# Kernel tuning notes

Measured on AMD Instinct MI355X. Metric: run time of the kernel, lower is better.

## Reference

```python
import jax, jax.numpy as jnp
import numpy as np

IN, H, OUT, R, E, B = 4096, 4096, 4096, 512, 4, 64
TOT = R * IN + H * R + R * H + OUT * R  # 8388608


def setup_inputs() -> dict:
    key = jax.random.key(0)
    ks = jax.random.split(key, 7)
    s = 0.02
    x = jax.random.normal(ks[0], (B, IN), jnp.float32)
    scores = jax.random.uniform(ks[1], (E,), jnp.float32)
    delta = jax.random.normal(ks[2], (E, 1, TOT), jnp.float32) * s
    # single shared expert's base weights (all experts alias the same module)
    W1 = jax.random.normal(ks[3], (R, IN), jnp.float32) * s   # hidden_layer_u.weight
    W2 = jax.random.normal(ks[4], (H, R), jnp.float32) * s    # hidden_layer_v.weight
    W3 = jax.random.normal(ks[5], (R, H), jnp.float32) * s    # output_layer_u.weight
    W4 = jax.random.normal(ks[6], (OUT, R), jnp.float32) * s  # output_layer_v.weight
    return {"x": x, "scores": scores, "delta": delta, "W1": W1, "W2": W2, "W3": W3, "W4": W4}


def reference(x, scores, delta, W1, W2, W3, W4):
    # slice flat per-expert deltas into the four weight deltas
    d = delta[:, 0, :]                                   # [E, TOT]
    j = 0
    d1 = d[:, j:j + R * IN].reshape(E, R, IN); j += R * IN
    d2 = d[:, j:j + H * R].reshape(E, H, R);   j += H * R
    d3 = d[:, j:j + R * H].reshape(E, R, H);   j += R * H
    d4 = d[:, j:j + OUT * R].reshape(E, OUT, R)
    Wa = W1[None] + d1   # [E, R, IN]
    Wb = W2[None] + d2   # [E, H, R]
    Wc = W3[None] + d3   # [E, R, H]
    Wd = W4[None] + d4   # [E, OUT, R]
    h = jnp.einsum('bi,eri->ebr', x, Wa)                 # F.linear with W1+d1
    h = jnp.einsum('ebr,ehr->ebh', h, Wb)                # F.linear with W2+d2
    h = jax.nn.relu(h)
    h = jnp.einsum('ebh,erh->ebr', h, Wc)                # F.linear with W3+d3
    h = jnp.einsum('ebr,eor->ebo', h, Wd)                # F.linear with W4+d4
    return jnp.einsum('ebo,e->bo', h, scores)            # score-weighted sum over experts
```

## Files before the change

### kernel.cpp

```cpp
#include <hip/hip_runtime.h>
#include <hip/hip_bf16.h>

#define E_N 4
#define B_N 64
#define IN_N 4096
#define H_N 4096
#define R_N 512
#define OUT_N 4096
#define TOT_N 8388608

typedef float f32x4 __attribute__((ext_vector_type(4)));
typedef short bf16x8 __attribute__((ext_vector_type(8)));

__device__ __forceinline__ unsigned short f2bf_bits(float f) {
    return __builtin_bit_cast(unsigned short, __float2bfloat16(f));
}
__device__ __forceinline__ float bfbits2f(unsigned short u) {
    return __builtin_bit_cast(float, ((unsigned)u) << 16);
}

__device__ __forceinline__ void stage16(const void* g, void* l) {
    __builtin_amdgcn_global_load_lds(
        (const __attribute__((address_space(1))) void*)g,
        (__attribute__((address_space(3))) void*)l, 16, 0, 0);
}

template<int K_TOT, int N_TOT, int KS, bool A_SHARED, bool RELU, bool OUT_BF16>
__global__ __launch_bounds__(256, 2)
void gemm_layer(const __hip_bfloat16* __restrict__ A, const float* __restrict__ W,
                const float* __restrict__ D, float* __restrict__ OutF,
                __hip_bfloat16* __restrict__ OutB)
{
    constexpr int KCH = K_TOT / KS;
    constexpr int NT = N_TOT / 32;
    constexpr int NTILES = KCH / 64;
    constexpr int BUFSZ = 24576;
    __shared__ __align__(16) char smem[2 * BUFSZ];

    const int bid = blockIdx.x;
    const int ks = bid % KS;
    const int nt = (bid / KS) % NT;
    const int e  = bid / (KS * NT);
    const int tid = threadIdx.x;
    const int l  = tid & 63;
    const int w  = tid >> 6;
    const int wn = w & 1;
    const int wm = w >> 1;
    const int lr = l & 15;
    const int lk = (l >> 4) << 3;

    const float* Wb = W + (size_t)(nt * 32) * K_TOT + ks * KCH;
    const float* Db = D + (size_t)e * TOT_N + (size_t)(nt * 32) * K_TOT + ks * KCH;
    const __hip_bfloat16* Ab = A + (A_SHARED ? (size_t)0 : (size_t)e * B_N * K_TOT)
                                 + ks * KCH;

    const char* gsrc[6];
    int loff[6];
    int kstep[6];
    #pragma unroll
    for (int i = 0; i < 6; ++i) {
        const int q = w * 6 + i;
        if (q < 8) {
            const int off = q * 1024 + l * 16;
            const int row = off >> 8;
            const int kb  = off & 255;
            gsrc[i] = (const char*)(Wb + (size_t)row * K_TOT) + (kb ^ ((row & 7) << 4));
            loff[i] = q * 1024;
            kstep[i] = 4;
        } else if (q < 16) {
            const int c = q - 8;
            const int off = c * 1024 + l * 16;
            const int row = off >> 8;
            const int kb  = off & 255;
            gsrc[i] = (const char*)(Db + (size_t)row * K_TOT) + (kb ^ ((row & 7) << 4));
            loff[i] = 8192 + c * 1024;
            kstep[i] = 4;
        } else {
            const int c = q - 16;
            const int off = c * 1024 + l * 16;
            const int row = off >> 7;
            const int kb  = off & 127;
            gsrc[i] = (const char*)(Ab + (size_t)row * K_TOT) + (kb ^ ((row & 7) << 4));
            loff[i] = 16384 + c * 1024;
            kstep[i] = 2;
        }
    }

    f32x4 acc[2] = {};
    const int wrow = wn * 16 + lr;
    const int wswz = (wrow & 7) << 4;
    const int arow0 = wm * 32 + lr;
    const int aswz = (arow0 & 7) << 4;

    #pragma unroll
    for (int i = 0; i < 6; ++i)
        stage16(gsrc[i], smem + loff[i]);
    __syncthreads();

    for (int t = 0; t < NTILES; ++t) {
        if (t + 1 < NTILES) {
            const int kk = (t + 1) * 64;
            char* b = smem + ((t + 1) & 1) * BUFSZ;
            #pragma unroll
            for (int i = 0; i < 6; ++i)
                stage16(gsrc[i] + kk * kstep[i], b + loff[i]);
        }

        const char* buf = smem + (t & 1) * BUFSZ;
        #pragma unroll
        for (int inner = 0; inner < 2; ++inner) {
            const int b0 = (inner * 32 + lk) * 4;
            const char* wrp = buf + wrow * 256;
            const char* drp = buf + 8192 + wrow * 256;
            f32x4 w0 = *(const f32x4*)(wrp + ((b0)      ^ wswz));
            f32x4 w1 = *(const f32x4*)(wrp + ((b0 + 16) ^ wswz));
            f32x4 d0 = *(const f32x4*)(drp + ((b0)      ^ wswz));
            f32x4 d1 = *(const f32x4*)(drp + ((b0 + 16) ^ wswz));
            f32x4 s0 = w0 + d0;
            f32x4 s1 = w1 + d1;
            bf16x8 bhi, blo;
            #pragma unroll
            for (int j = 0; j < 4; ++j) {
                unsigned short h0 = f2bf_bits(s0[j]);
                bhi[j] = (short)h0;
                blo[j] = (short)f2bf_bits(s0[j] - bfbits2f(h0));
                unsigned short h1 = f2bf_bits(s1[j]);
                bhi[j + 4] = (short)h1;
                blo[j + 4] = (short)f2bf_bits(s1[j] - bfbits2f(h1));
            }
            const int ab = (inner * 32 + lk) * 2;
            #pragma unroll
            for (int mf = 0; mf < 2; ++mf) {
                const int ar = arow0 + mf * 16;
                const char* arp = buf + 16384 + ar * 128;
                bf16x8 af = *(const bf16x8*)(arp + (ab ^ aswz));
                acc[mf] = __builtin_amdgcn_mfma_f32_16x16x32_bf16(af, bhi, acc[mf], 0, 0, 0);
                acc[mf] = __builtin_amdgcn_mfma_f32_16x16x32_bf16(af, blo, acc[mf], 0, 0, 0);
            }
        }
        __syncthreads();
    }

    const int rb = (l >> 4) * 4;
    const int nrow = nt * 32 + wrow;
    #pragma unroll
    for (int j = 0; j < 2; ++j) {
        #pragma unroll
        for (int i = 0; i < 4; ++i) {
            const int row = wm * 32 + j * 16 + rb + i;
            float v = acc[j][i];
            if (RELU) v = fmaxf(v, 0.0f);
            if (OUT_BF16) {
                OutB[(size_t)e * B_N * N_TOT + (size_t)row * N_TOT + nrow] =
                    __float2bfloat16(v);
            } else {
                OutF[(size_t)(e * KS + ks) * B_N * N_TOT + (size_t)row * N_TOT + nrow] = v;
            }
        }
    }
}

template<int KS, int BN>
__global__ __launch_bounds__(256)
void reduce_ks_bf16(const float* __restrict__ P, __hip_bfloat16* __restrict__ H)
{
    const int gt = blockIdx.x * 256 + threadIdx.x;
    const int e = gt / BN;
    const int r = gt - e * BN;
    const float* base = P + (size_t)e * KS * BN + r;
    float s = 0.0f;
    #pragma unroll
    for (int k = 0; k < KS; ++k) s += base[(size_t)k * BN];
    H[gt] = __float2bfloat16(s);
}

__global__ __launch_bounds__(256)
void convert_bf16(const float* __restrict__ X, __hip_bfloat16* __restrict__ Xb)
{
    const int gt = blockIdx.x * 256 + threadIdx.x;
    const int idx = gt * 2;
    const float2 v = *(const float2*)(X + idx);
    const unsigned u = ((unsigned)f2bf_bits(v.y) << 16) | f2bf_bits(v.x);
    *(unsigned*)((char*)Xb + (size_t)idx * 2) = u;
}

__global__ __launch_bounds__(256)
void reduce_experts(const float* __restrict__ P, const float* __restrict__ scores,
                    float* __restrict__ out)
{
    const int gt = blockIdx.x * 256 + threadIdx.x;
    const int idx = gt * 2;
    float2 acc = {0.0f, 0.0f};
    #pragma unroll
    for (int e = 0; e < E_N; ++e) {
        const float2 v = *(const float2*)(P + (size_t)e * (B_N * OUT_N) + idx);
        const float s = scores[e];
        acc.x += s * v.x;
        acc.y += s * v.y;
    }
    *(float2*)(out + idx) = acc;
}

extern "C" void kernel_launch(void* const* d_in, const int* in_sizes, int n_in,
                              void* d_out, int out_size, void* d_ws, size_t ws_size,
                              hipStream_t stream)
{
    const float* x      = (const float*)d_in[0];
    const float* scores = (const float*)d_in[1];
    const float* delta  = (const float*)d_in[2];
    const float* W1     = (const float*)d_in[3];
    const float* W2     = (const float*)d_in[4];
    const float* W3     = (const float*)d_in[5];
    const float* W4     = (const float*)d_in[6];
    float* out = (float*)d_out;

    char* ws = (char*)d_ws;
    __hip_bfloat16* xb  = (__hip_bfloat16*)(ws);
    __hip_bfloat16* h1b = (__hip_bfloat16*)(ws + 524288);
    __hip_bfloat16* h2b = (__hip_bfloat16*)(ws + 786432);
    __hip_bfloat16* h3b = (__hip_bfloat16*)(ws + 2883584);
    float* P1 = (float*)(ws + 3145728);
    float* P3 = (float*)(ws + 7340032);
    float* P4 = (float*)(ws + 11534336);

    const float* d1 = delta;
    const float* d2 = d1 + (size_t)R_N * IN_N;
    const float* d3 = d2 + (size_t)H_N * R_N;
    const float* d4 = d3 + (size_t)R_N * H_N;

    convert_bf16<<<dim3(B_N * IN_N / 2 / 256), dim3(256), 0, stream>>>(x, xb);

    gemm_layer<IN_N, R_N, 8, true, false, false>
        <<<dim3(E_N * (R_N / 32) * 8), dim3(256), 0, stream>>>(xb, W1, d1, P1, nullptr);
    reduce_ks_bf16<8, B_N * R_N>
        <<<dim3(E_N * B_N * R_N / 256), dim3(256), 0, stream>>>(P1, h1b);

    gemm_layer<R_N, H_N, 1, false, true, true>
        <<<dim3(E_N * (H_N / 32)), dim3(256), 0, stream>>>(h1b, W2, d2, nullptr, h2b);

    gemm_layer<H_N, R_N, 8, false, false, false>
        <<<dim3(E_N * (R_N / 32) * 8), dim3(256), 0, stream>>>(h2b, W3, d3, P3, nullptr);
    reduce_ks_bf16<8, B_N * R_N>
        <<<dim3(E_N * B_N * R_N / 256), dim3(256), 0, stream>>>(P3, h3b);

    gemm_layer<R_N, OUT_N, 1, false, false, false>
        <<<dim3(E_N * (OUT_N / 32)), dim3(256), 0, stream>>>(h3b, W4, d4, P4, nullptr);

    reduce_experts<<<dim3(B_N * OUT_N / 2 / 256), dim3(256), 0, stream>>>(P4, scores, out);
}
```

Measured before the change: 51.43 us.

## Fold expert score sum into last layer GEMM over concatenated expert K

Scales each expert's layer-3 activations by its score while reducing split-K partials. The activations are written into a layout where experts are concatenated along K. The last layer then becomes a single GEMM with K=E*R that writes the output directly. This removes the per-expert fp32 partial output buffer and the separate expert-reduction kernel. The trade-off is that only 128 blocks run the last layer, with a longer K loop, which may underuse the GPU, and bf16 rounding of the score-scaled activations changes numerics slightly.

```diff
diff --git a/kernel.cpp b/kernel.cpp
--- a/kernel.cpp
+++ b/kernel.cpp
@@ -160,6 +160,129 @@
     }
 }
 
+__global__ __launch_bounds__(256, 2)
+void gemm_l4(const __hip_bfloat16* __restrict__ A, const float* __restrict__ W,
+             const float* __restrict__ D, float* __restrict__ Out)
+{
+    constexpr int KT = E_N * R_N;
+    constexpr int NTILES = KT / 64;
+    constexpr int BUFSZ = 24576;
+    __shared__ __align__(16) char smem[2 * BUFSZ];
+
+    const int nt = blockIdx.x;
+    const int tid = threadIdx.x;
+    const int l  = tid & 63;
+    const int w  = tid >> 6;
+    const int wn = w & 1;
+    const int wm = w >> 1;
+    const int lr = l & 15;
+    const int lk = (l >> 4) << 3;
+
+    const char* gsrc[6];
+    int loff[6];
+    int cls[6];
+    #pragma unroll
+    for (int i = 0; i < 6; ++i) {
+        const int q = w * 6 + i;
+        if (q < 8) {
+            const int off = q * 1024 + l * 16;
+            const int row = off >> 8;
+            const int kb  = (off & 255) ^ (((off >> 8) & 7) << 4);
+            gsrc[i] = (const char*)(W + (size_t)(nt * 32 + row) * R_N) + kb;
+            loff[i] = q * 1024;
+            cls[i] = 0;
+        } else if (q < 16) {
+            const int c = q - 8;
+            const int off = c * 1024 + l * 16;
+            const int row = off >> 8;
+            const int kb  = (off & 255) ^ (((off >> 8) & 7) << 4);
+            gsrc[i] = (const char*)(D + (size_t)(nt * 32 + row) * R_N) + kb;
+            loff[i] = 8192 + c * 1024;
+            cls[i] = 1;
+        } else {
+            const int c = q - 16;
+            const int off = c * 1024 + l * 16;
+            const int row = off >> 7;
+            const int kb  = (off & 127) ^ (((off >> 7) & 7) << 4);
+            gsrc[i] = (const char*)(A + (size_t)row * KT) + kb;
+            loff[i] = 16384 + c * 1024;
+            cls[i] = 2;
+        }
+    }
+
+    f32x4 acc[2] = {};
+    const int wrow = wn * 16 + lr;
+    const int wswz = (wrow & 7) << 4;
+    const int arow0 = wm * 32 + lr;
+    const int aswz = (arow0 & 7) << 4;
+
+    auto toff = [](int c, int kk) -> size_t {
+        if (c == 0) return (size_t)(kk & 511) * 4;
+        if (c == 1) return ((size_t)(kk >> 9) * (size_t)TOT_N + (kk & 511)) * 4;
+        return (size_t)kk * 2;
+    };
+
+    #pragma unroll
+    for (int i = 0; i < 6; ++i)
+        stage16(gsrc[i] + toff(cls[i], 0), smem + loff[i]);
+    __syncthreads();
+
+    for (int t = 0; t < NTILES; ++t) {
+        if (t + 1 < NTILES) {
+            const int kk = (t + 1) * 64;
+            char* b = smem + ((t + 1) & 1) * BUFSZ;
+            #pragma unroll
+            for (int i = 0; i < 6; ++i)
+                stage16(gsrc[i] + toff(cls[i], kk), b + loff[i]);
+        }
+
+        const char* buf = smem + (t & 1) * BUFSZ;
+        #pragma unroll
+        for (int inner = 0; inner < 2; ++inner) {
+            const int b0 = (inner * 32 + lk) * 4;
+            const char* wrp = buf + wrow * 256;
+            const char* drp = buf + 8192 + wrow * 256;
+            f32x4 w0 = *(const f32x4*)(wrp + ((b0)      ^ wswz));
+            f32x4 w1 = *(const f32x4*)(wrp + ((b0 + 16) ^ wswz));
+            f32x4 d0 = *(const f32x4*)(drp + ((b0)      ^ wswz));
+            f32x4 d1 = *(const f32x4*)(drp + ((b0 + 16) ^ wswz));
+            f32x4 s0 = w0 + d0;
+            f32x4 s1 = w1 + d1;
+            bf16x8 bhi, blo;
+            #pragma unroll
+            for (int j = 0; j < 4; ++j) {
+                unsigned short h0 = f2bf_bits(s0[j]);
+                bhi[j] = (short)h0;
+                blo[j] = (short)f2bf_bits(s0[j] - bfbits2f(h0));
+                unsigned short h1 = f2bf_bits(s1[j]);
+                bhi[j + 4] = (short)h1;
+                blo[j + 4] = (short)f2bf_bits(s1[j] - bfbits2f(h1));
+            }
+            const int ab = (inner * 32 + lk) * 2;
+            #pragma unroll
+            for (int mf = 0; mf < 2; ++mf) {
+                const int ar = arow0 + mf * 16;
+                const char* arp = buf + 16384 + ar * 128;
+                bf16x8 af = *(const bf16x8*)(arp + (ab ^ aswz));
+                acc[mf] = __builtin_amdgcn_mfma_f32_16x16x32_bf16(af, bhi, acc[mf], 0, 0, 0);
+                acc[mf] = __builtin_amdgcn_mfma_f32_16x16x32_bf16(af, blo, acc[mf], 0, 0, 0);
+            }
+        }
+        __syncthreads();
+    }
+
+    const int rb = (l >> 4) * 4;
+    const int nrow = nt * 32 + wrow;
+    #pragma unroll
+    for (int j = 0; j < 2; ++j) {
+        #pragma unroll
+        for (int i = 0; i < 4; ++i) {
+            const int row = wm * 32 + j * 16 + rb + i;
+            Out[(size_t)row * OUT_N + nrow] = acc[j][i];
+        }
+    }
+}
+
 template<int KS, int BN>
 __global__ __launch_bounds__(256)
 void reduce_ks_bf16(const float* __restrict__ P, __hip_bfloat16* __restrict__ H)
@@ -175,6 +298,23 @@
 }
 
 __global__ __launch_bounds__(256)
+void reduce_ks_scaled(const float* __restrict__ P, const float* __restrict__ scores,
+                      __hip_bfloat16* __restrict__ H)
+{
+    const int gt = blockIdx.x * 256 + threadIdx.x;
+    const int e = gt >> 15;
+    const int rem = gt & 32767;
+    const int b = rem >> 9;
+    const int r = rem & 511;
+    const float* base = P + (size_t)e * 8 * 32768 + rem;
+    float s = 0.0f;
+    #pragma unroll
+    for (int k = 0; k < 8; ++k) s += base[(size_t)k * 32768];
+    const float v = scores[e] * __bfloat162float(__float2bfloat16(s));
+    H[(size_t)b * (E_N * R_N) + e * R_N + r] = __float2bfloat16(v);
+}
+
+__global__ __launch_bounds__(256)
 void convert_bf16(const float* __restrict__ X, __hip_bfloat16* __restrict__ Xb)
 {
     const int gt = blockIdx.x * 256 + threadIdx.x;
@@ -182,23 +322,6 @@
     const float2 v = *(const float2*)(X + idx);
     const unsigned u = ((unsigned)f2bf_bits(v.y) << 16) | f2bf_bits(v.x);
     *(unsigned*)((char*)Xb + (size_t)idx * 2) = u;
-}
-
-__global__ __launch_bounds__(256)
-void reduce_experts(const float* __restrict__ P, const float* __restrict__ scores,
-                    float* __restrict__ out)
-{
-    const int gt = blockIdx.x * 256 + threadIdx.x;
-    const int idx = gt * 2;
-    float2 acc = {0.0f, 0.0f};
-    #pragma unroll
-    for (int e = 0; e < E_N; ++e) {
-        const float2 v = *(const float2*)(P + (size_t)e * (B_N * OUT_N) + idx);
-        const float s = scores[e];
-        acc.x += s * v.x;
-        acc.y += s * v.y;
-    }
-    *(float2*)(out + idx) = acc;
 }
 
 extern "C" void kernel_launch(void* const* d_in, const int* in_sizes, int n_in,
@@ -218,10 +341,9 @@
     __hip_bfloat16* xb  = (__hip_bfloat16*)(ws);
     __hip_bfloat16* h1b = (__hip_bfloat16*)(ws + 524288);
     __hip_bfloat16* h2b = (__hip_bfloat16*)(ws + 786432);
-    __hip_bfloat16* h3b = (__hip_bfloat16*)(ws + 2883584);
+    __hip_bfloat16* h3s = (__hip_bfloat16*)(ws + 2883584);
     float* P1 = (float*)(ws + 3145728);
     float* P3 = (float*)(ws + 7340032);
-    float* P4 = (float*)(ws + 11534336);
 
     const float* d1 = delta;
     const float* d2 = d1 + (size_t)R_N * IN_N;
@@ -240,11 +362,7 @@
 
     gemm_layer<H_N, R_N, 8, false, false, false>
         <<<dim3(E_N * (R_N / 32) * 8), dim3(256), 0, stream>>>(h2b, W3, d3, P3, nullptr);
-    reduce_ks_bf16<8, B_N * R_N>
-        <<<dim3(E_N * B_N * R_N / 256), dim3(256), 0, stream>>>(P3, h3b);
-
-    gemm_layer<R_N, OUT_N, 1, false, false, false>
-        <<<dim3(E_N * (OUT_N / 32)), dim3(256), 0, stream>>>(h3b, W4, d4, P4, nullptr);
-
-    reduce_experts<<<dim3(B_N * OUT_N / 2 / 256), dim3(256), 0, stream>>>(P4, scores, out);
-}
+    reduce_ks_scaled<<<dim3(E_N * B_N * R_N / 256), dim3(256), 0, stream>>>(P3, scores, h3s);
+
+    gemm_l4<<<dim3(OUT_N / 32), dim3(256), 0, stream>>>(h3s, W4, d4, out);
+}
```

After: 63.82 us. 24.1% more time.
